# Optimization experiments

Hardware: AMD Instinct MI355X
Metric: run time of the kernel (lower is better)

The kernel has to match this reference:

```python
import jax, jax.numpy as jnp
import numpy as np
from jax import lax

LN_EPS = 1e-5

def _conv1d(h, w, b):
    # h: [N, L, Cin], w: [Cout, Cin, K] (torch Conv1d layout), padding=1
    out = lax.conv_general_dilated(h, w, window_strides=(1,), padding=[(1, 1)],
                                   dimension_numbers=("NWC", "OIW", "NWC"))
    return out + b

def _layer_norm(h, g, b):
    m = jnp.mean(h, axis=-1, keepdims=True)
    v = jnp.mean((h - m) ** 2, axis=-1, keepdims=True)
    return (h - m) * lax.rsqrt(v + LN_EPS) * g + b

def setup_inputs() -> dict:
    key = jax.random.key(0)
    ks = jax.random.split(key, 8)
    N, L, D, F = 32, 512, 384, 256
    return {
        "x": jax.random.normal(ks[0], (N, L, D), jnp.float32),
        "conv1_w": jax.random.normal(ks[1], (F, D, 3), jnp.float32) * 0.05,
        "conv1_b": jnp.zeros((F,), jnp.float32),
        "ln1_g": jnp.ones((F,), jnp.float32),
        "ln1_b": jnp.zeros((F,), jnp.float32),
        "conv2_w": jax.random.normal(ks[2], (F, F, 3), jnp.float32) * 0.05,
        "conv2_b": jnp.zeros((F,), jnp.float32),
        "ln2_g": jnp.ones((F,), jnp.float32),
        "ln2_b": jnp.zeros((F,), jnp.float32),
        "lin_w": jax.random.normal(ks[3], (F,), jnp.float32) * 0.05,
        "lin_b": jnp.zeros((), jnp.float32),
        "target": jax.random.randint(ks[4], (N, L), 0, 8, dtype=jnp.int32),
        "mel_max_length": 2048,
    }

def reference(x, conv1_w, conv1_b, ln1_g, ln1_b, conv2_w, conv2_b, ln2_g, ln2_b,
              lin_w, lin_b, target, mel_max_length):
    # Duration predictor (dropout is identity at inference)
    h = jax.nn.relu(_layer_norm(_conv1d(x, conv1_w, conv1_b), ln1_g, ln1_b))
    h = jax.nn.relu(_layer_norm(_conv1d(h, conv2_w, conv2_b), ln2_g, ln2_b))
    duration_predictor_output = jnp.einsum("nlf,f->nl", h, lin_w) + lin_b  # [N, L]

    # LR: frame t copies phoneme j iff cumsum(dur)[:j] <= t < cumsum(dur)[:j+1]
    # (equivalent to the one-hot alignment matmul, padded to mel_max_length)
    N, L, D = x.shape
    T = mel_max_length
    cums = jnp.cumsum(target, axis=-1)                      # [N, L]
    frames = jnp.arange(T, dtype=cums.dtype)                # [T]
    idx = jax.vmap(lambda c: jnp.searchsorted(c, frames, side="right"))(cums)  # [N, T]
    valid = frames[None, :] < cums[:, -1:]                  # frames beyond total are zero
    gathered = jnp.take_along_axis(x, jnp.clip(idx, 0, L - 1)[:, :, None], axis=1)
    output = gathered * valid[:, :, None].astype(x.dtype)   # [N, T, D]
    return output, duration_predictor_output
```

## Files before the change

### kernel.cpp

```cpp
#include <hip/hip_runtime.h>
#include <hip/hip_bf16.h>

#define NB   32
#define TMEL 2048

typedef unsigned short u16;
typedef short s8v __attribute__((ext_vector_type(8)));
typedef float f4v __attribute__((ext_vector_type(4)));
typedef u16 u16x8 __attribute__((ext_vector_type(8)));

static __device__ __forceinline__ u16 f2bf(float v) {
    __hip_bfloat16 h = __float2bfloat16(v);
    return *(u16*)&h;
}

__global__ __launch_bounds__(256) void prep_kernel(
    const float* __restrict__ x,
    const float* __restrict__ w1,
    const float* __restrict__ w2,
    const int*   __restrict__ target,
    u16* __restrict__ xb,
    u16* __restrict__ Wt1,
    u16* __restrict__ Wt2,
    int* __restrict__ idxv,
    u16* __restrict__ zbuf)
{
    __shared__ int c[512];
    const int b = blockIdx.x, tid = threadIdx.x;
    if (b == 0 && tid < 8) {
        u16x8 z = {0, 0, 0, 0, 0, 0, 0, 0};
        *(u16x8*)(zbuf + tid * 8) = z;
    }
    if (b < 3072) {
        int i = b * 256 + tid;
        const f4v* p = (const f4v*)(x + (size_t)i * 8);
        f4v v0 = p[0], v1 = p[1];
        float vv[8] = {v0[0], v0[1], v0[2], v0[3], v1[0], v1[1], v1[2], v1[3]};
        u16x8 r;
        #pragma unroll
        for (int j = 0; j < 8; j++) r[j] = f2bf(vv[j]);
        *(u16x8*)(xb + (size_t)i * 8) = r;
    } else if (b < 3072 + 1152) {
        const int K = 1152, DIN = 384;
        int e = (b - 3072) * 256 + tid;
        int f = e / K;
        int rem = e - f * K;
        int kc = rem / DIN;
        int d = rem - kc * DIN;
        Wt1[e] = f2bf(w1[f * K + d * 3 + kc]);
    } else if (b < 4992) {
        const int K = 768, DIN = 256;
        int e = (b - 4224) * 256 + tid;
        int f = e / K;
        int rem = e - f * K;
        int kc = rem / DIN;
        int d = rem - kc * DIN;
        Wt2[e] = f2bf(w2[f * K + d * 3 + kc]);
    } else {
        const int n = b - 4992;
        c[tid]       = target[n * 512 + tid];
        c[tid + 256] = target[n * 512 + 256 + tid];
        __syncthreads();
        for (int off = 1; off < 512; off <<= 1) {
            int v0 = (tid       >= off) ? c[tid       - off] : 0;
            int v1 = (tid + 256 >= off) ? c[tid + 256 - off] : 0;
            __syncthreads();
            c[tid]       += v0;
            c[tid + 256] += v1;
            __syncthreads();
        }
        const int total = c[511];
        for (int t = tid; t < TMEL; t += 256) {
            int lo = 0, hi = 512;
            while (lo < hi) {
                int mid = (lo + hi) >> 1;
                if (c[mid] <= t) lo = mid + 1; else hi = mid;
            }
            idxv[n * TMEL + t] = (t < total) ? min(lo, 511) : -1;
        }
    }
}

template<int DIN, int MODE>
__global__ __launch_bounds__(256, 2) void conv_mfma_kernel(
    const u16* __restrict__ Ain,
    const u16* __restrict__ Wt,
    const float* __restrict__ cb,
    const float* __restrict__ g,
    const float* __restrict__ bb,
    const float* __restrict__ lw,
    const float* __restrict__ lbp,
    const u16* __restrict__ zbuf,
    void* __restrict__ outp)
{
    const int K = 3 * DIN, NT = K / 64;
    __shared__ __align__(128) char AsB[2][32 * 128];
    __shared__ __align__(128) char BsB[2][256 * 128];
    __shared__ float redS[32 * 4];
    __shared__ float redQ[32 * 4];
    __shared__ float redP[32 * 4];

    const int tid  = threadIdx.x;
    const int lane = tid & 63, wc = tid >> 6;
    const int lr = lane & 15, q4 = lane >> 4;
    const int m0 = blockIdx.x * 32;
    const int n  = m0 >> 9, l0 = m0 & 511;

    f4v acc[2][4];
    #pragma unroll
    for (int mi = 0; mi < 2; mi++)
        #pragma unroll
        for (int ni = 0; ni < 4; ni++) acc[mi][ni] = {0.f, 0.f, 0.f, 0.f};

    const int a_r    = tid >> 3;
    const int a_slot = (tid & 7) ^ (a_r & 7);
    const int b_r    = tid >> 3;
    const int b_slot = (tid & 7) ^ (b_r & 7);

    const int aoff0 = (lr) * 128;
    const int aoff1 = (16 + lr) * 128;
    int boff[4];
    #pragma unroll
    for (int ni = 0; ni < 4; ni++) boff[ni] = (64 * wc + 16 * ni + lr) * 128;
    const int slot0 = ((q4)     ^ (lr & 7)) << 4;
    const int slot1 = ((q4 | 4) ^ (lr & 7)) << 4;

    auto stage = [&](int buf, int t) {
        const int k0 = t * 64;
        const int kc = k0 / DIN;
        const int d0 = k0 - kc * DIN;
        const int lp = l0 + a_r + kc - 1;
        const u16* asrc = (lp >= 0 && lp < 512)
            ? (Ain + ((size_t)((n << 9) + lp)) * DIN + d0 + a_slot * 8)
            : zbuf;
        __builtin_amdgcn_global_load_lds(
            (const __attribute__((address_space(1))) void*)asrc,
            (__attribute__((address_space(3))) void*)(AsB[buf] + tid * 16), 16, 0, 0);
        const u16* bsrc = Wt + (size_t)b_r * K + k0 + b_slot * 8;
        #pragma unroll
        for (int q = 0; q < 8; q++) {
            __builtin_amdgcn_global_load_lds(
                (const __attribute__((address_space(1))) void*)(bsrc + (size_t)q * 32 * K),
                (__attribute__((address_space(3))) void*)(BsB[buf] + q * 4096 + tid * 16),
                16, 0, 0);
        }
    };

    auto compute = [&](int buf) {
        #pragma unroll
        for (int kk = 0; kk < 2; kk++) {
            const int sl = kk ? slot1 : slot0;
            s8v a0 = *(const s8v*)(AsB[buf] + aoff0 + sl);
            s8v a1 = *(const s8v*)(AsB[buf] + aoff1 + sl);
            s8v b0 = *(const s8v*)(BsB[buf] + boff[0] + sl);
            s8v b1 = *(const s8v*)(BsB[buf] + boff[1] + sl);
            s8v b2 = *(const s8v*)(BsB[buf] + boff[2] + sl);
            s8v b3 = *(const s8v*)(BsB[buf] + boff[3] + sl);
            acc[0][0] = __builtin_amdgcn_mfma_f32_16x16x32_bf16(a0, b0, acc[0][0], 0, 0, 0);
            acc[0][1] = __builtin_amdgcn_mfma_f32_16x16x32_bf16(a0, b1, acc[0][1], 0, 0, 0);
            acc[0][2] = __builtin_amdgcn_mfma_f32_16x16x32_bf16(a0, b2, acc[0][2], 0, 0, 0);
            acc[0][3] = __builtin_amdgcn_mfma_f32_16x16x32_bf16(a0, b3, acc[0][3], 0, 0, 0);
            acc[1][0] = __builtin_amdgcn_mfma_f32_16x16x32_bf16(a1, b0, acc[1][0], 0, 0, 0);
            acc[1][1] = __builtin_amdgcn_mfma_f32_16x16x32_bf16(a1, b1, acc[1][1], 0, 0, 0);
            acc[1][2] = __builtin_amdgcn_mfma_f32_16x16x32_bf16(a1, b2, acc[1][2], 0, 0, 0);
            acc[1][3] = __builtin_amdgcn_mfma_f32_16x16x32_bf16(a1, b3, acc[1][3], 0, 0, 0);
        }
    };

    stage(0, 0);
    __syncthreads();
    int cur = 0;
    for (int t = 0; t < NT; ++t) {
        if (t + 1 < NT) stage(cur ^ 1, t + 1);
        compute(cur);
        __syncthreads();
        cur ^= 1;
    }

    float cbv[4], gv[4], bbv[4], lwv[4];
    int col[4];
    #pragma unroll
    for (int ni = 0; ni < 4; ni++) {
        col[ni] = 64 * wc + 16 * ni + lr;
        cbv[ni] = cb[col[ni]]; gv[ni] = g[col[ni]]; bbv[ni] = bb[col[ni]];
        if (MODE == 1) lwv[ni] = lw[col[ni]];
    }

    float sv[2][4], sq[2][4];
    #pragma unroll
    for (int mi = 0; mi < 2; mi++)
        #pragma unroll
        for (int reg = 0; reg < 4; reg++) {
            float s = 0.f, q = 0.f;
            #pragma unroll
            for (int ni = 0; ni < 4; ni++) {
                float v = acc[mi][ni][reg] + cbv[ni];
                s += v; q += v * v;
            }
            #pragma unroll
            for (int msk = 1; msk < 16; msk <<= 1) {
                s += __shfl_xor(s, msk);
                q += __shfl_xor(q, msk);
            }
            sv[mi][reg] = s; sq[mi][reg] = q;
        }
    if (lr == 0) {
        #pragma unroll
        for (int mi = 0; mi < 2; mi++)
            #pragma unroll
            for (int reg = 0; reg < 4; reg++) {
                int rl = 16 * mi + 4 * q4 + reg;
                redS[rl * 4 + wc] = sv[mi][reg];
                redQ[rl * 4 + wc] = sq[mi][reg];
            }
    }
    __syncthreads();

    float mean_[2][4], rs_[2][4];
    #pragma unroll
    for (int mi = 0; mi < 2; mi++)
        #pragma unroll
        for (int reg = 0; reg < 4; reg++) {
            int rl = 16 * mi + 4 * q4 + reg;
            float4 ps = *(float4*)&redS[rl * 4];
            float4 pq = *(float4*)&redQ[rl * 4];
            float mean = (ps.x + ps.y + ps.z + ps.w) * (1.f / 256.f);
            float var  = (pq.x + pq.y + pq.z + pq.w) * (1.f / 256.f) - mean * mean;
            mean_[mi][reg] = mean;
            rs_[mi][reg]   = rsqrtf(var + 1e-5f);
        }

    if (MODE == 0) {
        u16* hout = (u16*)outp;
        #pragma unroll
        for (int mi = 0; mi < 2; mi++)
            #pragma unroll
            for (int reg = 0; reg < 4; reg++) {
                int rl = 16 * mi + 4 * q4 + reg;
                #pragma unroll
                for (int ni = 0; ni < 4; ni++) {
                    float v = acc[mi][ni][reg] + cbv[ni];
                    float o = fmaxf(0.f, (v - mean_[mi][reg]) * rs_[mi][reg] * gv[ni] + bbv[ni]);
                    hout[(size_t)(m0 + rl) * 256 + col[ni]] = f2bf(o);
                }
            }
    } else {
        float pp[2][4];
        #pragma unroll
        for (int mi = 0; mi < 2; mi++)
            #pragma unroll
            for (int reg = 0; reg < 4; reg++) {
                float p = 0.f;
                #pragma unroll
                for (int ni = 0; ni < 4; ni++) {
                    float v = acc[mi][ni][reg] + cbv[ni];
                    float o = fmaxf(0.f, (v - mean_[mi][reg]) * rs_[mi][reg] * gv[ni] + bbv[ni]);
                    p += o * lwv[ni];
                }
                #pragma unroll
                for (int msk = 1; msk < 16; msk <<= 1) p += __shfl_xor(p, msk);
                pp[mi][reg] = p;
            }
        if (lr == 0) {
            #pragma unroll
            for (int mi = 0; mi < 2; mi++)
                #pragma unroll
                for (int reg = 0; reg < 4; reg++) {
                    int rl = 16 * mi + 4 * q4 + reg;
                    redP[rl * 4 + wc] = pp[mi][reg];
                }
        }
        __syncthreads();
        if (tid < 32) {
            float* dpo = (float*)outp;
            float4 p4 = *(float4*)&redP[tid * 4];
            dpo[m0 + tid] = p4.x + p4.y + p4.z + p4.w + lbp[0];
        }
    }
}

__global__ void lr_gather_kernel(const float* __restrict__ x,
                                 const int* __restrict__ idxv,
                                 float* __restrict__ out) {
    int gid = blockIdx.x * 256 + threadIdx.x;
    int f4  = gid % 48;
    int row = gid / 48;
    int n   = row >> 11;
    int ie  = idxv[row];
    f4v v0 = {0.f, 0.f, 0.f, 0.f}, v1 = v0;
    if (ie >= 0) {
        const float* src = &x[((size_t)(n << 9) + ie) * 384];
        v0 = *(const f4v*)&src[f4 * 4];
        v1 = *(const f4v*)&src[(f4 + 48) * 4];
    }
    float* dst = &out[(size_t)row * 384];
    __builtin_nontemporal_store(v0, (f4v*)&dst[f4 * 4]);
    __builtin_nontemporal_store(v1, (f4v*)&dst[(f4 + 48) * 4]);
}

extern "C" void kernel_launch(void* const* d_in, const int* in_sizes, int n_in,
                              void* d_out, int out_size, void* d_ws, size_t ws_size,
                              hipStream_t stream) {
    const float* x   = (const float*)d_in[0];
    const float* w1  = (const float*)d_in[1];
    const float* b1  = (const float*)d_in[2];
    const float* g1  = (const float*)d_in[3];
    const float* bb1 = (const float*)d_in[4];
    const float* w2  = (const float*)d_in[5];
    const float* b2  = (const float*)d_in[6];
    const float* g2  = (const float*)d_in[7];
    const float* bb2 = (const float*)d_in[8];
    const float* lw  = (const float*)d_in[9];
    const float* lb  = (const float*)d_in[10];
    const int* target = (const int*)d_in[11];

    char* wsb  = (char*)d_ws;
    u16*  zbuf = (u16*)wsb;
    u16*  Wt1  = (u16*)(wsb + 128);
    u16*  Wt2  = (u16*)(wsb + 128 + 589824);
    u16*  xb   = (u16*)(wsb + 128 + 589824 + 393216);
    int*  idxv = (int*)(wsb + 128 + 589824 + 393216 + 12582912);

    float* out0 = (float*)d_out;
    float* dpo  = out0 + (size_t)32 * 2048 * 384;
    u16* h1 = (u16*)d_out;

    prep_kernel<<<5024, 256, 0, stream>>>(x, w1, w2, target, xb, Wt1, Wt2, idxv, zbuf);

    conv_mfma_kernel<384, 0><<<512, 256, 0, stream>>>(
        xb, Wt1, b1, g1, bb1, nullptr, nullptr, zbuf, (void*)h1);
    conv_mfma_kernel<256, 1><<<512, 256, 0, stream>>>(
        h1, Wt2, b2, g2, bb2, lw, lb, zbuf, (void*)dpo);

    lr_gather_kernel<<<12288, 256, 0, stream>>>(x, idxv, out0);
}
```

Measured before the change: 77.84 us.

## Fuse LR gather into conv kernels and convert x to bf16 on the fly

Removes the separate x-to-bf16 conversion pass by having conv1 load fp32 x and convert it while staging into LDS. The LR gather kernel is removed and its rows are split between the two conv launches as extra blocks, interleaved with the conv blocks, so the memory-bound copy overlaps with the MFMA work. h1 moves from the output buffer into workspace, since gather blocks now write the output at the same time. The trade-off is that conv1's A-tile staging becomes a register load-convert-store path instead of a direct global-to-LDS load, and gather blocks share the launch with heavier conv blocks.

```diff
diff --git a/kernel.cpp b/kernel.cpp
--- a/kernel.cpp
+++ b/kernel.cpp
@@ -15,11 +15,9 @@
 }
 
 __global__ __launch_bounds__(256) void prep_kernel(
-    const float* __restrict__ x,
     const float* __restrict__ w1,
     const float* __restrict__ w2,
     const int*   __restrict__ target,
-    u16* __restrict__ xb,
     u16* __restrict__ Wt1,
     u16* __restrict__ Wt2,
     int* __restrict__ idxv,
@@ -31,33 +29,24 @@
         u16x8 z = {0, 0, 0, 0, 0, 0, 0, 0};
         *(u16x8*)(zbuf + tid * 8) = z;
     }
-    if (b < 3072) {
-        int i = b * 256 + tid;
-        const f4v* p = (const f4v*)(x + (size_t)i * 8);
-        f4v v0 = p[0], v1 = p[1];
-        float vv[8] = {v0[0], v0[1], v0[2], v0[3], v1[0], v1[1], v1[2], v1[3]};
-        u16x8 r;
-        #pragma unroll
-        for (int j = 0; j < 8; j++) r[j] = f2bf(vv[j]);
-        *(u16x8*)(xb + (size_t)i * 8) = r;
-    } else if (b < 3072 + 1152) {
+    if (b < 1152) {
         const int K = 1152, DIN = 384;
-        int e = (b - 3072) * 256 + tid;
+        int e = b * 256 + tid;
         int f = e / K;
         int rem = e - f * K;
         int kc = rem / DIN;
         int d = rem - kc * DIN;
         Wt1[e] = f2bf(w1[f * K + d * 3 + kc]);
-    } else if (b < 4992) {
+    } else if (b < 1920) {
         const int K = 768, DIN = 256;
-        int e = (b - 4224) * 256 + tid;
+        int e = (b - 1152) * 256 + tid;
         int f = e / K;
         int rem = e - f * K;
         int kc = rem / DIN;
         int d = rem - kc * DIN;
         Wt2[e] = f2bf(w2[f * K + d * 3 + kc]);
     } else {
-        const int n = b - 4992;
+        const int n = b - 1920;
         c[tid]       = target[n * 512 + tid];
         c[tid + 256] = target[n * 512 + 256 + tid];
         __syncthreads();
@@ -81,9 +70,9 @@
     }
 }
 
-template<int DIN, int MODE>
-__global__ __launch_bounds__(256, 2) void conv_mfma_kernel(
-    const u16* __restrict__ Ain,
+template<int DIN, int MODE, int ASRC>
+__global__ __launch_bounds__(256, 2) void conv_gather_kernel(
+    const void* __restrict__ Ainp,
     const u16* __restrict__ Wt,
     const float* __restrict__ cb,
     const float* __restrict__ g,
@@ -91,211 +80,239 @@
     const float* __restrict__ lw,
     const float* __restrict__ lbp,
     const u16* __restrict__ zbuf,
-    void* __restrict__ outp)
+    void* __restrict__ outp,
+    const float* __restrict__ xf,
+    const int* __restrict__ idxv,
+    float* __restrict__ out0,
+    int gbase)
 {
-    const int K = 3 * DIN, NT = K / 64;
-    __shared__ __align__(128) char AsB[2][32 * 128];
-    __shared__ __align__(128) char BsB[2][256 * 128];
-    __shared__ float redS[32 * 4];
-    __shared__ float redQ[32 * 4];
-    __shared__ float redP[32 * 4];
-
-    const int tid  = threadIdx.x;
-    const int lane = tid & 63, wc = tid >> 6;
-    const int lr = lane & 15, q4 = lane >> 4;
-    const int m0 = blockIdx.x * 32;
-    const int n  = m0 >> 9, l0 = m0 & 511;
-
-    f4v acc[2][4];
-    #pragma unroll
-    for (int mi = 0; mi < 2; mi++)
-        #pragma unroll
-        for (int ni = 0; ni < 4; ni++) acc[mi][ni] = {0.f, 0.f, 0.f, 0.f};
-
-    const int a_r    = tid >> 3;
-    const int a_slot = (tid & 7) ^ (a_r & 7);
-    const int b_r    = tid >> 3;
-    const int b_slot = (tid & 7) ^ (b_r & 7);
-
-    const int aoff0 = (lr) * 128;
-    const int aoff1 = (16 + lr) * 128;
-    int boff[4];
-    #pragma unroll
-    for (int ni = 0; ni < 4; ni++) boff[ni] = (64 * wc + 16 * ni + lr) * 128;
-    const int slot0 = ((q4)     ^ (lr & 7)) << 4;
-    const int slot1 = ((q4 | 4) ^ (lr & 7)) << 4;
-
-    auto stage = [&](int buf, int t) {
-        const int k0 = t * 64;
-        const int kc = k0 / DIN;
-        const int d0 = k0 - kc * DIN;
-        const int lp = l0 + a_r + kc - 1;
-        const u16* asrc = (lp >= 0 && lp < 512)
-            ? (Ain + ((size_t)((n << 9) + lp)) * DIN + d0 + a_slot * 8)
-            : zbuf;
-        __builtin_amdgcn_global_load_lds(
-            (const __attribute__((address_space(1))) void*)asrc,
-            (__attribute__((address_space(3))) void*)(AsB[buf] + tid * 16), 16, 0, 0);
-        const u16* bsrc = Wt + (size_t)b_r * K + k0 + b_slot * 8;
-        #pragma unroll
-        for (int q = 0; q < 8; q++) {
-            __builtin_amdgcn_global_load_lds(
-                (const __attribute__((address_space(1))) void*)(bsrc + (size_t)q * 32 * K),
-                (__attribute__((address_space(3))) void*)(BsB[buf] + q * 4096 + tid * 16),
-                16, 0, 0);
-        }
-    };
-
-    auto compute = [&](int buf) {
-        #pragma unroll
-        for (int kk = 0; kk < 2; kk++) {
-            const int sl = kk ? slot1 : slot0;
-            s8v a0 = *(const s8v*)(AsB[buf] + aoff0 + sl);
-            s8v a1 = *(const s8v*)(AsB[buf] + aoff1 + sl);
-            s8v b0 = *(const s8v*)(BsB[buf] + boff[0] + sl);
-            s8v b1 = *(const s8v*)(BsB[buf] + boff[1] + sl);
-            s8v b2 = *(const s8v*)(BsB[buf] + boff[2] + sl);
-            s8v b3 = *(const s8v*)(BsB[buf] + boff[3] + sl);
-            acc[0][0] = __builtin_amdgcn_mfma_f32_16x16x32_bf16(a0, b0, acc[0][0], 0, 0, 0);
-            acc[0][1] = __builtin_amdgcn_mfma_f32_16x16x32_bf16(a0, b1, acc[0][1], 0, 0, 0);
-            acc[0][2] = __builtin_amdgcn_mfma_f32_16x16x32_bf16(a0, b2, acc[0][2], 0, 0, 0);
-            acc[0][3] = __builtin_amdgcn_mfma_f32_16x16x32_bf16(a0, b3, acc[0][3], 0, 0, 0);
-            acc[1][0] = __builtin_amdgcn_mfma_f32_16x16x32_bf16(a1, b0, acc[1][0], 0, 0, 0);
-            acc[1][1] = __builtin_amdgcn_mfma_f32_16x16x32_bf16(a1, b1, acc[1][1], 0, 0, 0);
-            acc[1][2] = __builtin_amdgcn_mfma_f32_16x16x32_bf16(a1, b2, acc[1][2], 0, 0, 0);
-            acc[1][3] = __builtin_amdgcn_mfma_f32_16x16x32_bf16(a1, b3, acc[1][3], 0, 0, 0);
-        }
-    };
-
-    stage(0, 0);
-    __syncthreads();
-    int cur = 0;
-    for (int t = 0; t < NT; ++t) {
-        if (t + 1 < NT) stage(cur ^ 1, t + 1);
-        compute(cur);
+    const int tid = threadIdx.x;
+    {
+        const int b = blockIdx.x;
+        int role, rid;
+        if (b < 1024) { role = b & 1; rid = b >> 1; }
+        else          { role = 1;     rid = b - 512; }
+
+        if (role == 1) {
+            int t  = rid * 256 + tid;
+            int j  = t % 48;
+            int rr = t / 48;
+            #pragma unroll
+            for (int h = 0; h < 2; h++) {
+                int row = gbase + rr + h * 16384;
+                int n   = row >> 11;
+                int ie  = idxv[row];
+                f4v v0 = {0.f, 0.f, 0.f, 0.f}, v1 = v0;
+                if (ie >= 0) {
+                    const float* src = &xf[((size_t)(n << 9) + ie) * 384];
+                    v0 = *(const f4v*)&src[j * 4];
+                    v1 = *(const f4v*)&src[(j + 48) * 4];
+                }
+                float* dst = &out0[(size_t)row * 384];
+                __builtin_nontemporal_store(v0, (f4v*)&dst[j * 4]);
+                __builtin_nontemporal_store(v1, (f4v*)&dst[(j + 48) * 4]);
+            }
+            return;
+        }
+
+        const int K = 3 * DIN, NT = K / 64;
+        __shared__ __align__(128) char AsB[2][32 * 128];
+        __shared__ __align__(128) char BsB[2][256 * 128];
+        __shared__ float redS[32 * 4];
+        __shared__ float redQ[32 * 4];
+        __shared__ float redP[32 * 4];
+
+        const int lane = tid & 63, wc = tid >> 6;
+        const int lr = lane & 15, q4 = lane >> 4;
+        const int m0 = rid * 32;
+        const int n  = m0 >> 9, l0 = m0 & 511;
+
+        f4v acc[2][4];
+        #pragma unroll
+        for (int mi = 0; mi < 2; mi++)
+            #pragma unroll
+            for (int ni = 0; ni < 4; ni++) acc[mi][ni] = {0.f, 0.f, 0.f, 0.f};
+
+        const int a_r    = tid >> 3;
+        const int a_slot = (tid & 7) ^ (a_r & 7);
+        const int b_r    = tid >> 3;
+        const int b_slot = (tid & 7) ^ (b_r & 7);
+
+        const int aoff0 = (lr) * 128;
+        const int aoff1 = (16 + lr) * 128;
+        int boff[4];
+        #pragma unroll
+        for (int ni = 0; ni < 4; ni++) boff[ni] = (64 * wc + 16 * ni + lr) * 128;
+        const int slot0 = ((q4)     ^ (lr & 7)) << 4;
+        const int slot1 = ((q4 | 4) ^ (lr & 7)) << 4;
+
+        auto stage = [&](int buf, int t) {
+            const int k0 = t * 64;
+            const int kc = k0 / DIN;
+            const int d0 = k0 - kc * DIN;
+            const int lp = l0 + a_r + kc - 1;
+            if (ASRC == 0) {
+                f4v v0 = {0.f, 0.f, 0.f, 0.f}, v1 = v0;
+                if (lp >= 0 && lp < 512) {
+                    const float* src = (const float*)Ainp
+                        + ((size_t)((n << 9) + lp)) * DIN + d0 + (tid & 7) * 8;
+                    v0 = *(const f4v*)src;
+                    v1 = *(const f4v*)(src + 4);
+                }
+                u16x8 r;
+                #pragma unroll
+                for (int jj = 0; jj < 4; jj++) { r[jj] = f2bf(v0[jj]); r[4 + jj] = f2bf(v1[jj]); }
+                *(u16x8*)(AsB[buf] + a_r * 128 + a_slot * 16) = r;
+            } else {
+                const u16* asrc = (lp >= 0 && lp < 512)
+                    ? ((const u16*)Ainp + ((size_t)((n << 9) + lp)) * DIN + d0 + a_slot * 8)
+                    : zbuf;
+                __builtin_amdgcn_global_load_lds(
+                    (const __attribute__((address_space(1))) void*)asrc,
+                    (__attribute__((address_space(3))) void*)(AsB[buf] + tid * 16), 16, 0, 0);
+            }
+            const u16* bsrc = Wt + (size_t)b_r * K + k0 + b_slot * 8;
+            #pragma unroll
+            for (int q = 0; q < 8; q++) {
+                __builtin_amdgcn_global_load_lds(
+                    (const __attribute__((address_space(1))) void*)(bsrc + (size_t)q * 32 * K),
+                    (__attribute__((address_space(3))) void*)(BsB[buf] + q * 4096 + tid * 16),
+                    16, 0, 0);
+            }
+        };
+
+        auto compute = [&](int buf) {
+            #pragma unroll
+            for (int kk = 0; kk < 2; kk++) {
+                const int sl = kk ? slot1 : slot0;
+                s8v a0 = *(const s8v*)(AsB[buf] + aoff0 + sl);
+                s8v a1 = *(const s8v*)(AsB[buf] + aoff1 + sl);
+                s8v b0 = *(const s8v*)(BsB[buf] + boff[0] + sl);
+                s8v b1 = *(const s8v*)(BsB[buf] + boff[1] + sl);
+                s8v b2 = *(const s8v*)(BsB[buf] + boff[2] + sl);
+                s8v b3 = *(const s8v*)(BsB[buf] + boff[3] + sl);
+                acc[0][0] = __builtin_amdgcn_mfma_f32_16x16x32_bf16(a0, b0, acc[0][0], 0, 0, 0);
+                acc[0][1] = __builtin_amdgcn_mfma_f32_16x16x32_bf16(a0, b1, acc[0][1], 0, 0, 0);
+                acc[0][2] = __builtin_amdgcn_mfma_f32_16x16x32_bf16(a0, b2, acc[0][2], 0, 0, 0);
+                acc[0][3] = __builtin_amdgcn_mfma_f32_16x16x32_bf16(a0, b3, acc[0][3], 0, 0, 0);
+                acc[1][0] = __builtin_amdgcn_mfma_f32_16x16x32_bf16(a1, b0, acc[1][0], 0, 0, 0);
+                acc[1][1] = __builtin_amdgcn_mfma_f32_16x16x32_bf16(a1, b1, acc[1][1], 0, 0, 0);
+                acc[1][2] = __builtin_amdgcn_mfma_f32_16x16x32_bf16(a1, b2, acc[1][2], 0, 0, 0);
+                acc[1][3] = __builtin_amdgcn_mfma_f32_16x16x32_bf16(a1, b3, acc[1][3], 0, 0, 0);
+            }
+        };
+
+        stage(0, 0);
         __syncthreads();
-        cur ^= 1;
-    }
-
-    float cbv[4], gv[4], bbv[4], lwv[4];
-    int col[4];
-    #pragma unroll
-    for (int ni = 0; ni < 4; ni++) {
-        col[ni] = 64 * wc + 16 * ni + lr;
-        cbv[ni] = cb[col[ni]]; gv[ni] = g[col[ni]]; bbv[ni] = bb[col[ni]];
-        if (MODE == 1) lwv[ni] = lw[col[ni]];
-    }
-
-    float sv[2][4], sq[2][4];
-    #pragma unroll
-    for (int mi = 0; mi < 2; mi++)
-        #pragma unroll
-        for (int reg = 0; reg < 4; reg++) {
-            float s = 0.f, q = 0.f;
-            #pragma unroll
-            for (int ni = 0; ni < 4; ni++) {
-                float v = acc[mi][ni][reg] + cbv[ni];
-                s += v; q += v * v;
-            }
-            #pragma unroll
-            for (int msk = 1; msk < 16; msk <<= 1) {
-                s += __shfl_xor(s, msk);
-                q += __shfl_xor(q, msk);
-            }
-            sv[mi][reg] = s; sq[mi][reg] = q;
-        }
-    if (lr == 0) {
+        int cur = 0;
+        for (int t = 0; t < NT; ++t) {
+            if (t + 1 < NT) stage(cur ^ 1, t + 1);
+            compute(cur);
+            __syncthreads();
+            cur ^= 1;
+        }
+
+        float cbv[4], gv[4], bbv[4], lwv[4];
+        int col[4];
+        #pragma unroll
+        for (int ni = 0; ni < 4; ni++) {
+            col[ni] = 64 * wc + 16 * ni + lr;
+            cbv[ni] = cb[col[ni]]; gv[ni] = g[col[ni]]; bbv[ni] = bb[col[ni]];
+            if (MODE == 1) lwv[ni] = lw[col[ni]];
+        }
+
+        float sv[2][4], sq[2][4];
+        #pragma unroll
+        for (int mi = 0; mi < 2; mi++)
+            #pragma unroll
+            for (int reg = 0; reg < 4; reg++) {
+                float s = 0.f, q = 0.f;
+                #pragma unroll
+                for (int ni = 0; ni < 4; ni++) {
+                    float v = acc[mi][ni][reg] + cbv[ni];
+                    s += v; q += v * v;
+                }
+                #pragma unroll
+                for (int msk = 1; msk < 16; msk <<= 1) {
+                    s += __shfl_xor(s, msk);
+                    q += __shfl_xor(q, msk);
+                }
+                sv[mi][reg] = s; sq[mi][reg] = q;
+            }
+        if (lr == 0) {
+            #pragma unroll
+            for (int mi = 0; mi < 2; mi++)
+                #pragma unroll
+                for (int reg = 0; reg < 4; reg++) {
+                    int rl = 16 * mi + 4 * q4 + reg;
+                    redS[rl * 4 + wc] = sv[mi][reg];
+                    redQ[rl * 4 + wc] = sq[mi][reg];
+                }
+        }
+        __syncthreads();
+
+        float mean_[2][4], rs_[2][4];
         #pragma unroll
         for (int mi = 0; mi < 2; mi++)
             #pragma unroll
             for (int reg = 0; reg < 4; reg++) {
                 int rl = 16 * mi + 4 * q4 + reg;
-                redS[rl * 4 + wc] = sv[mi][reg];
-                redQ[rl * 4 + wc] = sq[mi][reg];
-            }
-    }
-    __syncthreads();
-
-    float mean_[2][4], rs_[2][4];
-    #pragma unroll
-    for (int mi = 0; mi < 2; mi++)
-        #pragma unroll
-        for (int reg = 0; reg < 4; reg++) {
-            int rl = 16 * mi + 4 * q4 + reg;
-            float4 ps = *(float4*)&redS[rl * 4];
-            float4 pq = *(float4*)&redQ[rl * 4];
-            float mean = (ps.x + ps.y + ps.z + ps.w) * (1.f / 256.f);
-            float var  = (pq.x + pq.y + pq.z + pq.w) * (1.f / 256.f) - mean * mean;
-            mean_[mi][reg] = mean;
-            rs_[mi][reg]   = rsqrtf(var + 1e-5f);
-        }
-
-    if (MODE == 0) {
-        u16* hout = (u16*)outp;
-        #pragma unroll
-        for (int mi = 0; mi < 2; mi++)
-            #pragma unroll
-            for (int reg = 0; reg < 4; reg++) {
-                int rl = 16 * mi + 4 * q4 + reg;
-                #pragma unroll
-                for (int ni = 0; ni < 4; ni++) {
-                    float v = acc[mi][ni][reg] + cbv[ni];
-                    float o = fmaxf(0.f, (v - mean_[mi][reg]) * rs_[mi][reg] * gv[ni] + bbv[ni]);
-                    hout[(size_t)(m0 + rl) * 256 + col[ni]] = f2bf(o);
-                }
-            }
-    } else {
-        float pp[2][4];
-        #pragma unroll
-        for (int mi = 0; mi < 2; mi++)
-            #pragma unroll
-            for (int reg = 0; reg < 4; reg++) {
-                float p = 0.f;
-                #pragma unroll
-                for (int ni = 0; ni < 4; ni++) {
-                    float v = acc[mi][ni][reg] + cbv[ni];
-                    float o = fmaxf(0.f, (v - mean_[mi][reg]) * rs_[mi][reg] * gv[ni] + bbv[ni]);
-                    p += o * lwv[ni];
-                }
-                #pragma unroll
-                for (int msk = 1; msk < 16; msk <<= 1) p += __shfl_xor(p, msk);
-                pp[mi][reg] = p;
-            }
-        if (lr == 0) {
+                float4 ps = *(float4*)&redS[rl * 4];
+                float4 pq = *(float4*)&redQ[rl * 4];
+                float mean = (ps.x + ps.y + ps.z + ps.w) * (1.f / 256.f);
+                float var  = (pq.x + pq.y + pq.z + pq.w) * (1.f / 256.f) - mean * mean;
+                mean_[mi][reg] = mean;
+                rs_[mi][reg]   = rsqrtf(var + 1e-5f);
+            }
+
+        if (MODE == 0) {
+            u16* hout = (u16*)outp;
             #pragma unroll
             for (int mi = 0; mi < 2; mi++)
                 #pragma unroll
                 for (int reg = 0; reg < 4; reg++) {
                     int rl = 16 * mi + 4 * q4 + reg;
-                    redP[rl * 4 + wc] = pp[mi][reg];
-                }
-        }
-        __syncthreads();
-        if (tid < 32) {
-            float* dpo = (float*)outp;
-            float4 p4 = *(float4*)&redP[tid * 4];
-            dpo[m0 + tid] = p4.x + p4.y + p4.z + p4.w + lbp[0];
+                    #pragma unroll
+                    for (int ni = 0; ni < 4; ni++) {
+                        float v = acc[mi][ni][reg] + cbv[ni];
+                        float o = fmaxf(0.f, (v - mean_[mi][reg]) * rs_[mi][reg] * gv[ni] + bbv[ni]);
+                        hout[(size_t)(m0 + rl) * 256 + col[ni]] = f2bf(o);
+                    }
+                }
+        } else {
+            float pp[2][4];
+            #pragma unroll
+            for (int mi = 0; mi < 2; mi++)
+                #pragma unroll
+                for (int reg = 0; reg < 4; reg++) {
+                    float p = 0.f;
+                    #pragma unroll
+                    for (int ni = 0; ni < 4; ni++) {
+                        float v = acc[mi][ni][reg] + cbv[ni];
+                        float o = fmaxf(0.f, (v - mean_[mi][reg]) * rs_[mi][reg] * gv[ni] + bbv[ni]);
+                        p += o * lwv[ni];
+                    }
+                    #pragma unroll
+                    for (int msk = 1; msk < 16; msk <<= 1) p += __shfl_xor(p, msk);
+                    pp[mi][reg] = p;
+                }
+            if (lr == 0) {
+                #pragma unroll
+                for (int mi = 0; mi < 2; mi++)
+                    #pragma unroll
+                    for (int reg = 0; reg < 4; reg++) {
+                        int rl = 16 * mi + 4 * q4 + reg;
+                        redP[rl * 4 + wc] = pp[mi][reg];
+                    }
+            }
+            __syncthreads();
+            if (tid < 32) {
+                float* dpo = (float*)outp;
+                float4 p4 = *(float4*)&redP[tid * 4];
+                dpo[m0 + tid] = p4.x + p4.y + p4.z + p4.w + lbp[0];
+            }
         }
     }
-}
-
-__global__ void lr_gather_kernel(const float* __restrict__ x,
-                                 const int* __restrict__ idxv,
-                                 float* __restrict__ out) {
-    int gid = blockIdx.x * 256 + threadIdx.x;
-    int f4  = gid % 48;
-    int row = gid / 48;
-    int n   = row >> 11;
-    int ie  = idxv[row];
-    f4v v0 = {0.f, 0.f, 0.f, 0.f}, v1 = v0;
-    if (ie >= 0) {
-        const float* src = &x[((size_t)(n << 9) + ie) * 384];
-        v0 = *(const f4v*)&src[f4 * 4];
-        v1 = *(const f4v*)&src[(f4 + 48) * 4];
-    }
-    float* dst = &out[(size_t)row * 384];
-    __builtin_nontemporal_store(v0, (f4v*)&dst[f4 * 4]);
-    __builtin_nontemporal_store(v1, (f4v*)&dst[(f4 + 48) * 4]);
 }
 
 extern "C" void kernel_launch(void* const* d_in, const int* in_sizes, int n_in,
@@ -318,19 +335,19 @@
     u16*  zbuf = (u16*)wsb;
     u16*  Wt1  = (u16*)(wsb + 128);
     u16*  Wt2  = (u16*)(wsb + 128 + 589824);
-    u16*  xb   = (u16*)(wsb + 128 + 589824 + 393216);
-    int*  idxv = (int*)(wsb + 128 + 589824 + 393216 + 12582912);
+    u16*  h1   = (u16*)(wsb + 128 + 589824 + 393216);
+    int*  idxv = (int*)(wsb + 128 + 589824 + 393216 + 8388608);
 
     float* out0 = (float*)d_out;
     float* dpo  = out0 + (size_t)32 * 2048 * 384;
-    u16* h1 = (u16*)d_out;
-
-    prep_kernel<<<5024, 256, 0, stream>>>(x, w1, w2, target, xb, Wt1, Wt2, idxv, zbuf);
-
-    conv_mfma_kernel<384, 0><<<512, 256, 0, stream>>>(
-        xb, Wt1, b1, g1, bb1, nullptr, nullptr, zbuf, (void*)h1);
-    conv_mfma_kernel<256, 1><<<512, 256, 0, stream>>>(
-        h1, Wt2, b2, g2, bb2, lw, lb, zbuf, (void*)dpo);
-
-    lr_gather_kernel<<<12288, 256, 0, stream>>>(x, idxv, out0);
+
+    prep_kernel<<<1952, 256, 0, stream>>>(w1, w2, target, Wt1, Wt2, idxv, zbuf);
+
+    conv_gather_kernel<384, 0, 0><<<3584, 256, 0, stream>>>(
+        (const void*)x, Wt1, b1, g1, bb1, nullptr, nullptr, zbuf, (void*)h1,
+        x, idxv, out0, 0);
+
+    conv_gather_kernel<256, 1, 1><<<3584, 256, 0, stream>>>(
+        (const void*)h1, Wt2, b2, g2, bb2, lw, lb, zbuf, (void*)dpo,
+        x, idxv, out0, 32768);
 }
```

Result: slower. 110.8 us (+42.3%).
